# Performance work log

Measured on AMD Instinct MI355X. Metric: run time of the kernel, lower is better.

The kernel has to match this reference:

```python
import jax, jax.numpy as jnp
import numpy as np

D_MODEL = 1024
NUM_HEAD = 16
D_K = D_MODEL // NUM_HEAD


def setup_inputs() -> dict:
    key = jax.random.key(0)
    ks = jax.random.split(key, 9)
    s = 1.0 / np.sqrt(D_MODEL)
    x = jax.random.normal(ks[0], (2, 2048, D_MODEL), dtype=jnp.float32)
    Wq = jax.random.uniform(ks[1], (D_MODEL, D_MODEL), jnp.float32, -s, s)
    bq = jax.random.uniform(ks[2], (D_MODEL,), jnp.float32, -s, s)
    Wk = jax.random.uniform(ks[3], (D_MODEL, D_MODEL), jnp.float32, -s, s)
    bk = jax.random.uniform(ks[4], (D_MODEL,), jnp.float32, -s, s)
    Wv = jax.random.uniform(ks[5], (D_MODEL, D_MODEL), jnp.float32, -s, s)
    bv = jax.random.uniform(ks[6], (D_MODEL,), jnp.float32, -s, s)
    Wo = jax.random.uniform(ks[7], (D_MODEL, D_MODEL), jnp.float32, -s, s)
    bo = jax.random.uniform(ks[8], (D_MODEL,), jnp.float32, -s, s)
    return {"x": x, "Wq": Wq, "bq": bq, "Wk": Wk, "bk": bk,
            "Wv": Wv, "bv": bv, "Wo": Wo, "bo": bo}


def reference(x, Wq, bq, Wk, bk, Wv, bv, Wo, bo):
    b, n, d = x.shape
    h, dk = NUM_HEAD, D_K
    # Linear projections (torch Linear: x @ W.T + b)
    q = (x @ Wq.T + bq).reshape(b, n, h, dk).transpose(0, 2, 1, 3)  # [b,h,n,dk]
    k = (x @ Wk.T + bk).reshape(b, n, h, dk).transpose(0, 2, 1, 3)
    v = (x @ Wv.T + bv).reshape(b, n, h, dk).transpose(0, 2, 1, 3)
    scores = jnp.einsum('bhqd,bhkd->bhqk', q, k) / jnp.sqrt(jnp.float32(dk))
    attn = jax.nn.softmax(scores, axis=-1)  # [b,h,n,n]
    out = jnp.einsum('bhqk,bhkd->bhqd', attn, v)
    out = out.transpose(0, 2, 1, 3).reshape(b, n, d)
    return out @ Wo.T + bo
```

## Files before the change

kernel.cpp:

```cpp
#include <hip/hip_runtime.h>

#define BATCH   2
#define SEQ     2048
#define DMODEL  1024
#define NHEAD   16
#define DKH     64
#define MTOT    (BATCH*SEQ)
#define KDIM    DMODEL

#define XB    0u
#define WQB   (4u*1024u*1024u)
#define WKB   (5u*1024u*1024u)
#define WVB   (6u*1024u*1024u)
#define WOB   (7u*1024u*1024u)
#define QOFF  (8u*1024u*1024u)
#define KOFF  (12u*1024u*1024u)
#define VOFF  (16u*1024u*1024u)
#define OOFF  (20u*1024u*1024u)

typedef __bf16 bf16x8 __attribute__((ext_vector_type(8)));
typedef __bf16 bf16x4 __attribute__((ext_vector_type(4)));
typedef float  f32x4  __attribute__((ext_vector_type(4)));
typedef float  f32x16 __attribute__((ext_vector_type(16)));

__device__ __forceinline__ void async16(const __bf16* g, __bf16* l) {
  __builtin_amdgcn_global_load_lds(
      (const __attribute__((address_space(1))) void*)g,
      (__attribute__((address_space(3))) void*)l, 16, 0, 0);
}

__global__ __launch_bounds__(256) void cvt_fp32_bf16(
    const float* __restrict__ x,  const float* __restrict__ wq,
    const float* __restrict__ wk, const float* __restrict__ wv,
    const float* __restrict__ wo, __bf16* __restrict__ ws)
{
  const float* src; __bf16* dst; int n;
  switch (blockIdx.y) {
    case 0:  src = x;  dst = ws + XB;  n = 4 * 1024 * 1024; break;
    case 1:  src = wq; dst = ws + WQB; n = 1024 * 1024;     break;
    case 2:  src = wk; dst = ws + WKB; n = 1024 * 1024;     break;
    case 3:  src = wv; dst = ws + WVB; n = 1024 * 1024;     break;
    default: src = wo; dst = ws + WOB; n = 1024 * 1024;     break;
  }
  const int i = (blockIdx.x * 256 + threadIdx.x) * 8;
  if (i < n) {
    const float4 a = *(const float4*)(src + i);
    const float4 b = *(const float4*)(src + i + 4);
    bf16x8 o;
    o[0] = (__bf16)a.x; o[1] = (__bf16)a.y; o[2] = (__bf16)a.z; o[3] = (__bf16)a.w;
    o[4] = (__bf16)b.x; o[5] = (__bf16)b.y; o[6] = (__bf16)b.z; o[7] = (__bf16)b.w;
    *(bf16x8*)(dst + i) = o;
  }
}

__device__ __forceinline__ void gemm128_core(
    const __bf16* __restrict__ A, const __bf16* __restrict__ W,
    int m0, int n0, __bf16* lds, f32x4 (&acc)[4][4])
{
  __bf16* A_lds = lds;
  __bf16* B_lds = lds + 4096;
  const int t    = threadIdx.x;
  const int w    = t >> 6;
  const int lane = t & 63;
  const int ln15 = lane & 15;
  const int quad = lane >> 4;
  const int wr   = (w >> 1) << 6;
  const int wc   = (w & 1) << 6;

#pragma unroll
  for (int i = 0; i < 4; ++i)
#pragma unroll
    for (int j = 0; j < 4; ++j) acc[i][j] = (f32x4){0.f, 0.f, 0.f, 0.f};

  for (int kt = 0; kt < KDIM; kt += 32) {
    __syncthreads();
#pragma unroll
    for (int issue = 0; issue < 2; ++issue) {
      const int cbase = issue * 256 + (w << 6);
      const int c     = cbase + lane;
      const int row   = c >> 2;
      const int goff  = ((c & 3) ^ (row & 3)) << 3;
      async16(A + (size_t)(m0 + row) * KDIM + kt + goff, A_lds + cbase * 8);
      async16(W + (size_t)(n0 + row) * KDIM + kt + goff, B_lds + cbase * 8);
    }
    __syncthreads();

    bf16x8 af[4], bfr[4];
#pragma unroll
    for (int i = 0; i < 4; ++i) {
      const int row = wr + i * 16 + ln15;
      af[i] = *(const bf16x8*)&A_lds[row * 32 + ((quad ^ (row & 3)) << 3)];
    }
#pragma unroll
    for (int j = 0; j < 4; ++j) {
      const int row = wc + j * 16 + ln15;
      bfr[j] = *(const bf16x8*)&B_lds[row * 32 + ((quad ^ (row & 3)) << 3)];
    }
#pragma unroll
    for (int i = 0; i < 4; ++i)
#pragma unroll
      for (int j = 0; j < 4; ++j)
        acc[i][j] = __builtin_amdgcn_mfma_f32_16x16x32_bf16(af[i], bfr[j], acc[i][j], 0, 0, 0);
  }
}

__global__ __launch_bounds__(256) void qkv_gemm(
    const __bf16* __restrict__ X,
    const __bf16* __restrict__ Wq, const float* __restrict__ bq,
    const __bf16* __restrict__ Wk, const float* __restrict__ bk,
    const __bf16* __restrict__ Wv, const float* __restrict__ bv,
    __bf16* __restrict__ ws)
{
  __shared__ __align__(16) __bf16 lds[128 * 64];

  const int z = blockIdx.z;
  const __bf16* W    = (z == 0) ? Wq : (z == 1) ? Wk : Wv;
  const float*  bias = (z == 0) ? bq : (z == 1) ? bk : bv;
  __bf16* out = ws + ((z == 0) ? QOFF : (z == 1) ? KOFF : VOFF);
  const float scale = (z == 0) ? 0.125f * 1.44269504088896f : 1.0f;

  const int m0 = blockIdx.x * 128;
  const int n0 = blockIdx.y * 128;

  f32x4 acc[4][4];
  gemm128_core(X, W, m0, n0, lds, acc);

  const int t = threadIdx.x, w = t >> 6, lane = t & 63;
  const int ln15 = lane & 15, quad = lane >> 4;
  const int wr = (w >> 1) << 6, wc = (w & 1) << 6;

  float bj4[4];
#pragma unroll
  for (int j = 0; j < 4; ++j) bj4[j] = bias[n0 + wc + j * 16 + ln15];

  __syncthreads();
  __bf16* scr = lds + (w << 10);

  const int bb = m0 >> 11;
  const int s_base = (m0 & 2047) + wr;
  const int h = (n0 + wc) >> 6;

  if (z != 2) {
    const int rdrow = lane & 15, rdseg = lane >> 4;
#pragma unroll
    for (int i = 0; i < 4; ++i) {
#pragma unroll
      for (int j = 0; j < 4; ++j)
#pragma unroll
        for (int rr = 0; rr < 4; ++rr)
          scr[(quad * 4 + rr) * 64 + j * 16 + ln15] =
              (__bf16)((acc[i][j][rr] + bj4[j]) * scale);
      bf16x8 v0 = *(const bf16x8*)&scr[rdrow * 64 + rdseg * 16];
      bf16x8 v1 = *(const bf16x8*)&scr[rdrow * 64 + rdseg * 16 + 8];
      const int s = s_base + i * 16 + rdrow;
      __bf16* p = out + (((size_t)(bb * NHEAD + h)) * SEQ + s) * DKH + rdseg * 16;
      *(bf16x8*)p = v0;
      *(bf16x8*)&p[8] = v1;
    }
  } else {
#pragma unroll
    for (int i = 0; i < 4; ++i) {
#pragma unroll
      for (int j = 0; j < 4; ++j) {
        bf16x4 pk;
#pragma unroll
        for (int rr = 0; rr < 4; ++rr) pk[rr] = (__bf16)(acc[i][j][rr] + bj4[j]);
        *(bf16x4*)&scr[(j * 16 + ln15) * 16 + quad * 4] = pk;
      }
      bf16x8 c0 = *(const bf16x8*)&scr[lane * 16];
      bf16x8 c1 = *(const bf16x8*)&scr[lane * 16 + 8];
      __bf16* p = out + (((size_t)(bb * NHEAD + h)) * DKH + lane) * SEQ
                      + s_base + i * 16;
      *(bf16x8*)p = c0;
      *(bf16x8*)&p[8] = c1;
    }
  }
}

__global__ __launch_bounds__(256) void out_gemm(
    const __bf16* __restrict__ A, const __bf16* __restrict__ Wo,
    const float* __restrict__ bo, float* __restrict__ out)
{
  __shared__ __align__(16) __bf16 lds[6144];
  __bf16* A_lds = lds;
  __bf16* B_lds = lds + 2048;

  const int m0 = blockIdx.x * 64;
  const int n0 = blockIdx.y * 128;

  const int t = threadIdx.x, w = t >> 6, lane = t & 63;
  const int ln15 = lane & 15, quad = lane >> 4;

  f32x4 acc[4][2];
#pragma unroll
  for (int i = 0; i < 4; ++i)
#pragma unroll
    for (int j = 0; j < 2; ++j) acc[i][j] = (f32x4){0.f, 0.f, 0.f, 0.f};

  for (int kt = 0; kt < KDIM; kt += 32) {
    __syncthreads();
    {
      const int c = (w << 6) + lane;
      const int row = c >> 2;
      const int goff = ((c & 3) ^ (row & 3)) << 3;
      async16(A + (size_t)(m0 + row) * KDIM + kt + goff, A_lds + c * 8);
    }
#pragma unroll
    for (int issue = 0; issue < 2; ++issue) {
      const int cbase = issue * 256 + (w << 6);
      const int c = cbase + lane;
      const int row = c >> 2;
      const int goff = ((c & 3) ^ (row & 3)) << 3;
      async16(Wo + (size_t)(n0 + row) * KDIM + kt + goff, B_lds + cbase * 8);
    }
    __syncthreads();

    bf16x8 af[4], bfr[2];
#pragma unroll
    for (int i = 0; i < 4; ++i) {
      const int row = i * 16 + ln15;
      af[i] = *(const bf16x8*)&A_lds[row * 32 + ((quad ^ (row & 3)) << 3)];
    }
#pragma unroll
    for (int j = 0; j < 2; ++j) {
      const int row = (w << 5) + j * 16 + ln15;
      bfr[j] = *(const bf16x8*)&B_lds[row * 32 + ((quad ^ (row & 3)) << 3)];
    }
#pragma unroll
    for (int i = 0; i < 4; ++i)
#pragma unroll
      for (int j = 0; j < 2; ++j)
        acc[i][j] = __builtin_amdgcn_mfma_f32_16x16x32_bf16(af[i], bfr[j], acc[i][j], 0, 0, 0);
  }

  float bj2[2];
#pragma unroll
  for (int j = 0; j < 2; ++j) bj2[j] = bo[n0 + (w << 5) + j * 16 + ln15];

  __syncthreads();
  float* scrf = (float*)lds + (w << 9);

  const int rdrow = lane & 15, rdseg = lane >> 4;
#pragma unroll
  for (int i = 0; i < 4; ++i) {
#pragma unroll
    for (int j = 0; j < 2; ++j) {
      f32x4 v;
#pragma unroll
      for (int rr = 0; rr < 4; ++rr) v[rr] = acc[i][j][rr] + bj2[j];
      *(f32x4*)&scrf[(j * 16 + ln15) * 16 + quad * 4] = v;
    }
    const int m = m0 + i * 16 + rdrow;
    float* p = out + (size_t)m * DMODEL + n0 + (w << 5) + rdseg * 8;
#pragma unroll
    for (int cc = 0; cc < 2; ++cc) {
      f32x4 v;
#pragma unroll
      for (int e = 0; e < 4; ++e)
        v[e] = scrf[(rdseg * 8 + cc * 4 + e) * 16 + rdrow];
      *(f32x4*)&p[cc * 4] = v;
    }
  }
}

__global__ __launch_bounds__(256) void attn_kernel(
    const __bf16* __restrict__ Qb, const __bf16* __restrict__ Kb,
    const __bf16* __restrict__ Vtb, __bf16* __restrict__ Ob)
{
  __shared__ __align__(16) __bf16 QP[128 * 64];
  __shared__ __align__(16) __bf16 Ks[128 * 64];
  __shared__ __align__(16) __bf16 Vs[64 * 128];

  const int t = threadIdx.x, w = t >> 6, lane = t & 63;
  const int ln31 = lane & 31, hl = lane >> 5;
  const int bh = blockIdx.x;
  const int q0 = blockIdx.y * 128;
  const int b = bh >> 4, h = bh & 15;

  const __bf16* Qg = Qb + (size_t)bh * SEQ * DKH + (size_t)q0 * DKH;
  const __bf16* Kg = Kb + (size_t)bh * SEQ * DKH;
  const __bf16* Vg = Vtb + (size_t)bh * DKH * SEQ;

#pragma unroll
  for (int issue = 0; issue < 4; ++issue) {
    const int cbase = issue * 256 + (w << 6);
    const int c = cbase + lane;
    const int row = c >> 3;
    const int goff = ((c & 7) ^ (row & 7)) << 3;
    async16(Qg + (size_t)row * DKH + goff, QP + cbase * 8);
  }
  __syncthreads();

  const int qrow = (w << 5) + ln31;
  bf16x8 qf[4];
#pragma unroll
  for (int ks = 0; ks < 4; ++ks) {
    const int chunk = ((2 * ks + hl) ^ (qrow & 7));
    qf[ks] = *(const bf16x8*)&QP[qrow * 64 + (chunk << 3)];
  }

  float l_lane = 0.f;
  f32x16 o0, o1;
#pragma unroll
  for (int r = 0; r < 16; ++r) { o0[r] = 0.f; o1[r] = 0.f; }

  __bf16* Pw = QP + w * (32 * 64);

  for (int kt = 0; kt < SEQ; kt += 128) {
    __syncthreads();
#pragma unroll
    for (int issue = 0; issue < 4; ++issue) {
      const int cbase = issue * 256 + (w << 6);
      const int c = cbase + lane;
      const int krow = c >> 3;
      const int kgoff = ((c & 7) ^ (krow & 7)) << 3;
      async16(Kg + (size_t)(kt + krow) * DKH + kgoff, Ks + cbase * 8);
      const int vrow = c >> 4;
      const int vgoff = ((c & 15) ^ (vrow & 15)) << 3;
      async16(Vg + (size_t)vrow * SEQ + kt + vgoff, Vs + cbase * 8);
    }
    __syncthreads();

#pragma unroll
    for (int kb2 = 0; kb2 < 2; ++kb2) {
      f32x16 s0, s1;
#pragma unroll
      for (int r = 0; r < 16; ++r) { s0[r] = 0.f; s1[r] = 0.f; }
#pragma unroll
      for (int ks = 0; ks < 4; ++ks) {
        const int r0 = kb2 * 64 + ln31;
        const int r1 = kb2 * 64 + 32 + ln31;
        const int c0 = (((2 * ks + hl) ^ (r0 & 7)) << 3);
        const int c1 = (((2 * ks + hl) ^ (r1 & 7)) << 3);
        bf16x8 kf0 = *(const bf16x8*)&Ks[r0 * 64 + c0];
        bf16x8 kf1 = *(const bf16x8*)&Ks[r1 * 64 + c1];
        s0 = __builtin_amdgcn_mfma_f32_32x32x16_bf16(kf0, qf[ks], s0, 0, 0, 0);
        s1 = __builtin_amdgcn_mfma_f32_32x32x16_bf16(kf1, qf[ks], s1, 0, 0, 0);
      }

#pragma unroll
      for (int kb = 0; kb < 2; ++kb) {
        const f32x16& s = kb ? s1 : s0;
#pragma unroll
        for (int rg = 0; rg < 4; ++rg) {
          bf16x4 pk;
#pragma unroll
          for (int rr = 0; rr < 4; ++rr) {
            const float pv = __builtin_amdgcn_exp2f(s[rg * 4 + rr]);
            l_lane += pv;
            pk[rr] = (__bf16)pv;
          }
          const int g = kb * 4 + rg;
          *(bf16x4*)&Pw[ln31 * 64 + ((g ^ (ln31 & 7)) << 3) + hl * 4] = pk;
        }
      }

#pragma unroll
      for (int ks = 0; ks < 4; ++ks) {
        const int pg = (2 * ks + hl) ^ (ln31 & 7);
        bf16x8 pf = *(const bf16x8*)&Pw[ln31 * 64 + (pg << 3)];
        const int vchunk = kb2 * 8 + 2 * ks + hl;
        const int v0 = ln31;
        const int v1 = 32 + ln31;
        bf16x8 vf0 = *(const bf16x8*)&Vs[v0 * 128 + ((vchunk ^ (v0 & 15)) << 3)];
        bf16x8 vf1 = *(const bf16x8*)&Vs[v1 * 128 + ((vchunk ^ (v1 & 15)) << 3)];
        o0 = __builtin_amdgcn_mfma_f32_32x32x16_bf16(pf, vf0, o0, 0, 0, 0);
        o1 = __builtin_amdgcn_mfma_f32_32x32x16_bf16(pf, vf1, o1, 0, 0, 0);
      }
    }
  }

  l_lane += __shfl_xor(l_lane, 32);
  const float inv = 1.0f / l_lane;

#pragma unroll
  for (int r = 0; r < 16; ++r) {
    const int qi = (r & 3) + 8 * (r >> 2) + 4 * hl;
    const float iq = __shfl(inv, qi);
    const int q = q0 + (w << 5) + qi;
    __bf16* rowp = Ob + ((size_t)(b * SEQ + q)) * DMODEL + h * DKH;
    rowp[ln31]      = (__bf16)(o0[r] * iq);
    rowp[32 + ln31] = (__bf16)(o1[r] * iq);
  }
}

extern "C" void kernel_launch(void* const* d_in, const int* in_sizes, int n_in,
                              void* d_out, int out_size, void* d_ws, size_t ws_size,
                              hipStream_t stream)
{
  const float* x  = (const float*)d_in[0];
  const float* Wq = (const float*)d_in[1];
  const float* bq = (const float*)d_in[2];
  const float* Wk = (const float*)d_in[3];
  const float* bk = (const float*)d_in[4];
  const float* Wv = (const float*)d_in[5];
  const float* bv = (const float*)d_in[6];
  const float* Wo = (const float*)d_in[7];
  const float* bo = (const float*)d_in[8];
  float*  out = (float*)d_out;
  __bf16* ws  = (__bf16*)d_ws;

  cvt_fp32_bf16<<<dim3(2048, 5, 1), 256, 0, stream>>>(x, Wq, Wk, Wv, Wo, ws);

  qkv_gemm<<<dim3(MTOT / 128, DMODEL / 128, 3), 256, 0, stream>>>(
      ws + XB, ws + WQB, bq, ws + WKB, bk, ws + WVB, bv, ws);

  attn_kernel<<<dim3(BATCH * NHEAD, SEQ / 128), 256, 0, stream>>>(
      ws + QOFF, ws + KOFF, ws + VOFF, ws + OOFF);

  out_gemm<<<dim3(MTOT / 64, DMODEL / 128), 256, 0, stream>>>(
      ws + OOFF, ws + WOB, bo, out);
}
```

Baseline: 192.2 us.

## Split attention key tiles across two wave groups and keep P in registers

The attention kernel now runs 512 threads. Two groups of four waves each take half of every 128-key tile, and their partial outputs and row sums are combined through shared memory at the end. The softmax probabilities are packed to bf16 and rearranged between lanes with permlane32 swaps, so they are used directly as MFMA operands instead of round-tripping through shared memory. s_setprio hints are placed around the MFMA sections. The aim is more waves in flight to hide latency and less LDS traffic, at the cost of an extra reduction step and higher register pressure per block.

```diff
diff --git a/kernel.cpp b/kernel.cpp
--- a/kernel.cpp
+++ b/kernel.cpp
@@ -29,6 +29,15 @@
       (__attribute__((address_space(3))) void*)l, 16, 0, 0);
 }
 
+__device__ __forceinline__ unsigned cvtpk_bf16(float lo, float hi) {
+  unsigned r;
+  asm("v_cvt_pk_bf16_f32 %0, %1, %2" : "=v"(r) : "v"(lo), "v"(hi));
+  return r;
+}
+__device__ __forceinline__ void plswap(unsigned& a, unsigned& b) {
+  asm("v_permlane32_swap_b32 %0, %1" : "+v"(a), "+v"(b));
+}
+
 __global__ __launch_bounds__(256) void cvt_fp32_bf16(
     const float* __restrict__ x,  const float* __restrict__ wq,
     const float* __restrict__ wk, const float* __restrict__ wv,
@@ -263,27 +272,58 @@
   }
 }
 
-__global__ __launch_bounds__(256) void attn_kernel(
+__device__ __forceinline__ void softmax_frag(const f32x16& s, float& l,
+                                             bf16x8& pfa, bf16x8& pfb)
+{
+  float p[16];
+#pragma unroll
+  for (int r = 0; r < 16; ++r) {
+    p[r] = __builtin_amdgcn_exp2f(s[r]);
+    l += p[r];
+  }
+  unsigned A0 = cvtpk_bf16(p[0],  p[1]);
+  unsigned A1 = cvtpk_bf16(p[2],  p[3]);
+  unsigned B0 = cvtpk_bf16(p[4],  p[5]);
+  unsigned B1 = cvtpk_bf16(p[6],  p[7]);
+  unsigned C0 = cvtpk_bf16(p[8],  p[9]);
+  unsigned C1 = cvtpk_bf16(p[10], p[11]);
+  unsigned D0 = cvtpk_bf16(p[12], p[13]);
+  unsigned D1 = cvtpk_bf16(p[14], p[15]);
+  plswap(A0, B0);
+  plswap(A1, B1);
+  plswap(C0, D0);
+  plswap(C1, D1);
+  union { unsigned u[4]; bf16x8 v; } ua, ub;
+  ua.u[0] = A0; ua.u[1] = A1; ua.u[2] = B0; ua.u[3] = B1;
+  ub.u[0] = C0; ub.u[1] = C1; ub.u[2] = D0; ub.u[3] = D1;
+  pfa = ua.v;
+  pfb = ub.v;
+}
+
+__global__ __launch_bounds__(512, 4) void attn_kernel(
     const __bf16* __restrict__ Qb, const __bf16* __restrict__ Kb,
     const __bf16* __restrict__ Vtb, __bf16* __restrict__ Ob)
 {
-  __shared__ __align__(16) __bf16 QP[128 * 64];
-  __shared__ __align__(16) __bf16 Ks[128 * 64];
-  __shared__ __align__(16) __bf16 Vs[64 * 128];
+  __shared__ __align__(16) __bf16 smem[3 * 128 * 64];
+  __bf16* QP = smem;
+  __bf16* Ks = smem + 8192;
+  __bf16* Vs = smem + 16384;
 
   const int t = threadIdx.x, w = t >> 6, lane = t & 63;
   const int ln31 = lane & 31, hl = lane >> 5;
+  const int g  = w & 3;
+  const int kh = w >> 2;
   const int bh = blockIdx.x;
   const int q0 = blockIdx.y * 128;
-  const int b = bh >> 4, h = bh & 15;
+  const int bb = bh >> 4, hh = bh & 15;
 
   const __bf16* Qg = Qb + (size_t)bh * SEQ * DKH + (size_t)q0 * DKH;
   const __bf16* Kg = Kb + (size_t)bh * SEQ * DKH;
   const __bf16* Vg = Vtb + (size_t)bh * DKH * SEQ;
 
 #pragma unroll
-  for (int issue = 0; issue < 4; ++issue) {
-    const int cbase = issue * 256 + (w << 6);
+  for (int issue = 0; issue < 2; ++issue) {
+    const int cbase = issue * 512 + (w << 6);
     const int c = cbase + lane;
     const int row = c >> 3;
     const int goff = ((c & 7) ^ (row & 7)) << 3;
@@ -291,7 +331,7 @@
   }
   __syncthreads();
 
-  const int qrow = (w << 5) + ln31;
+  const int qrow = (g << 5) + ln31;
   bf16x8 qf[4];
 #pragma unroll
   for (int ks = 0; ks < 4; ++ks) {
@@ -304,13 +344,21 @@
 #pragma unroll
   for (int r = 0; r < 16; ++r) { o0[r] = 0.f; o1[r] = 0.f; }
 
-  __bf16* Pw = QP + w * (32 * 64);
+#define PVSTEP(KS, PF) do {                                                   \
+    const int vchunk = (kh << 3) + 2 * (KS) + hl;                             \
+    bf16x8 vf0 = *(const bf16x8*)&Vs[ln31 * 128 +                             \
+                                     ((vchunk ^ (ln31 & 15)) << 3)];          \
+    bf16x8 vf1 = *(const bf16x8*)&Vs[(32 + ln31) * 128 +                      \
+                                     ((vchunk ^ ((32 + ln31) & 15)) << 3)];   \
+    o0 = __builtin_amdgcn_mfma_f32_32x32x16_bf16(PF, vf0, o0, 0, 0, 0);       \
+    o1 = __builtin_amdgcn_mfma_f32_32x32x16_bf16(PF, vf1, o1, 0, 0, 0);       \
+  } while (0)
 
   for (int kt = 0; kt < SEQ; kt += 128) {
     __syncthreads();
 #pragma unroll
-    for (int issue = 0; issue < 4; ++issue) {
-      const int cbase = issue * 256 + (w << 6);
+    for (int issue = 0; issue < 2; ++issue) {
+      const int cbase = issue * 512 + (w << 6);
       const int c = cbase + lane;
       const int krow = c >> 3;
       const int kgoff = ((c & 7) ^ (krow & 7)) << 3;
@@ -321,66 +369,87 @@
     }
     __syncthreads();
 
-#pragma unroll
-    for (int kb2 = 0; kb2 < 2; ++kb2) {
-      f32x16 s0, s1;
-#pragma unroll
-      for (int r = 0; r < 16; ++r) { s0[r] = 0.f; s1[r] = 0.f; }
+    {
+      f32x16 s;
+#pragma unroll
+      for (int r = 0; r < 16; ++r) s[r] = 0.f;
+      const int kr = (kh << 6) + ln31;
+      __builtin_amdgcn_s_setprio(1);
 #pragma unroll
       for (int ks = 0; ks < 4; ++ks) {
-        const int r0 = kb2 * 64 + ln31;
-        const int r1 = kb2 * 64 + 32 + ln31;
-        const int c0 = (((2 * ks + hl) ^ (r0 & 7)) << 3);
-        const int c1 = (((2 * ks + hl) ^ (r1 & 7)) << 3);
-        bf16x8 kf0 = *(const bf16x8*)&Ks[r0 * 64 + c0];
-        bf16x8 kf1 = *(const bf16x8*)&Ks[r1 * 64 + c1];
-        s0 = __builtin_amdgcn_mfma_f32_32x32x16_bf16(kf0, qf[ks], s0, 0, 0, 0);
-        s1 = __builtin_amdgcn_mfma_f32_32x32x16_bf16(kf1, qf[ks], s1, 0, 0, 0);
+        bf16x8 kf = *(const bf16x8*)&Ks[kr * 64 + (((2 * ks + hl) ^ (kr & 7)) << 3)];
+        s = __builtin_amdgcn_mfma_f32_32x32x16_bf16(kf, qf[ks], s, 0, 0, 0);
       }
-
-#pragma unroll
-      for (int kb = 0; kb < 2; ++kb) {
-        const f32x16& s = kb ? s1 : s0;
-#pragma unroll
-        for (int rg = 0; rg < 4; ++rg) {
-          bf16x4 pk;
-#pragma unroll
-          for (int rr = 0; rr < 4; ++rr) {
-            const float pv = __builtin_amdgcn_exp2f(s[rg * 4 + rr]);
-            l_lane += pv;
-            pk[rr] = (__bf16)pv;
-          }
-          const int g = kb * 4 + rg;
-          *(bf16x4*)&Pw[ln31 * 64 + ((g ^ (ln31 & 7)) << 3) + hl * 4] = pk;
-        }
+      __builtin_amdgcn_s_setprio(0);
+      bf16x8 pa, pb;
+      softmax_frag(s, l_lane, pa, pb);
+      __builtin_amdgcn_s_setprio(1);
+      PVSTEP(0, pa);
+      PVSTEP(1, pb);
+      __builtin_amdgcn_s_setprio(0);
+    }
+    {
+      f32x16 s;
+#pragma unroll
+      for (int r = 0; r < 16; ++r) s[r] = 0.f;
+      const int kr = (kh << 6) + 32 + ln31;
+      __builtin_amdgcn_s_setprio(1);
+#pragma unroll
+      for (int ks = 0; ks < 4; ++ks) {
+        bf16x8 kf = *(const bf16x8*)&Ks[kr * 64 + (((2 * ks + hl) ^ (kr & 7)) << 3)];
+        s = __builtin_amdgcn_mfma_f32_32x32x16_bf16(kf, qf[ks], s, 0, 0, 0);
       }
-
-#pragma unroll
-      for (int ks = 0; ks < 4; ++ks) {
-        const int pg = (2 * ks + hl) ^ (ln31 & 7);
-        bf16x8 pf = *(const bf16x8*)&Pw[ln31 * 64 + (pg << 3)];
-        const int vchunk = kb2 * 8 + 2 * ks + hl;
-        const int v0 = ln31;
-        const int v1 = 32 + ln31;
-        bf16x8 vf0 = *(const bf16x8*)&Vs[v0 * 128 + ((vchunk ^ (v0 & 15)) << 3)];
-        bf16x8 vf1 = *(const bf16x8*)&Vs[v1 * 128 + ((vchunk ^ (v1 & 15)) << 3)];
-        o0 = __builtin_amdgcn_mfma_f32_32x32x16_bf16(pf, vf0, o0, 0, 0, 0);
-        o1 = __builtin_amdgcn_mfma_f32_32x32x16_bf16(pf, vf1, o1, 0, 0, 0);
-      }
-    }
-  }
-
+      __builtin_amdgcn_s_setprio(0);
+      bf16x8 pa, pb;
+      softmax_frag(s, l_lane, pa, pb);
+      __builtin_amdgcn_s_setprio(1);
+      PVSTEP(2, pa);
+      PVSTEP(3, pb);
+      __builtin_amdgcn_s_setprio(0);
+    }
+  }
+#undef PVSTEP
+
+  __syncthreads();
+  float* cmb = (float*)smem;
+  const int dsw = ln31 & 7;
   l_lane += __shfl_xor(l_lane, 32);
-  const float inv = 1.0f / l_lane;
-
-#pragma unroll
-  for (int r = 0; r < 16; ++r) {
-    const int qi = (r & 3) + 8 * (r >> 2) + 4 * hl;
-    const float iq = __shfl(inv, qi);
-    const int q = q0 + (w << 5) + qi;
-    __bf16* rowp = Ob + ((size_t)(b * SEQ + q)) * DMODEL + h * DKH;
-    rowp[ln31]      = (__bf16)(o0[r] * iq);
-    rowp[32 + ln31] = (__bf16)(o1[r] * iq);
+
+  if (w >= 4) {
+    float* base = cmb + (g << 11);
+#pragma unroll
+    for (int gg = 0; gg < 4; ++gg) {
+      const int qq = ((2 * gg + hl) ^ dsw) << 2;
+      f32x4 va, vb;
+#pragma unroll
+      for (int rr = 0; rr < 4; ++rr) { va[rr] = o0[4 * gg + rr]; vb[rr] = o1[4 * gg + rr]; }
+      *(f32x4*)&base[ln31 * 32 + qq]        = va;
+      *(f32x4*)&base[(32 + ln31) * 32 + qq] = vb;
+    }
+    if (hl == 0) cmb[8192 + (g << 5) + ln31] = l_lane;
+  }
+  __syncthreads();
+  if (w < 4) {
+    float* base = cmb + (g << 11);
+#pragma unroll
+    for (int gg = 0; gg < 4; ++gg) {
+      const int qq = ((2 * gg + hl) ^ dsw) << 2;
+      const f32x4 va = *(const f32x4*)&base[ln31 * 32 + qq];
+      const f32x4 vb = *(const f32x4*)&base[(32 + ln31) * 32 + qq];
+#pragma unroll
+      for (int rr = 0; rr < 4; ++rr) { o0[4 * gg + rr] += va[rr]; o1[4 * gg + rr] += vb[rr]; }
+    }
+    const float inv = 1.0f / (l_lane + cmb[8192 + (g << 5) + ln31]);
+
+#pragma unroll
+    for (int r = 0; r < 16; ++r) {
+      const int qi = (r & 3) + 8 * (r >> 2) + 4 * hl;
+      const float iq = __shfl(inv, qi);
+      const int q = q0 + (g << 5) + qi;
+      __bf16* rowp = Ob + ((size_t)(bb * SEQ + q)) * DMODEL + hh * DKH;
+      rowp[ln31]      = (__bf16)(o0[r] * iq);
+      rowp[32 + ln31] = (__bf16)(o1[r] * iq);
+    }
   }
 }
 
@@ -405,7 +474,7 @@
   qkv_gemm<<<dim3(MTOT / 128, DMODEL / 128, 3), 256, 0, stream>>>(
       ws + XB, ws + WQB, bq, ws + WKB, bk, ws + WVB, bv, ws);
 
-  attn_kernel<<<dim3(BATCH * NHEAD, SEQ / 128), 256, 0, stream>>>(
+  attn_kernel<<<dim3(BATCH * NHEAD, SEQ / 128), 512, 0, stream>>>(
       ws + QOFF, ws + KOFF, ws + VOFF, ws + OOFF);
 
   out_gemm<<<dim3(MTOT / 64, DMODEL / 128), 256, 0, stream>>>(
```

Result: faster. 186.7 us (-2.9%).
